# Kernel optimization log

Measured on AMD Instinct MI355X. Metric: run time of the kernel, lower is better.

## Reference

```python
import jax, jax.numpy as jnp
import numpy as np

D_MODEL = 1024
N_HEADS = 16
SEQ_LEN = 2048
BATCH = 2
NEG = -1.0e9


def sinusoidal_embeddings(seq_len, d_k):
    # Faithful to the torch version: row 0 is all zeros; even cols get sin,
    # odd cols get cos of position/theta (theta uses the SAME index j, not j//2).
    theta = 10000.0 ** (2.0 * jnp.arange(d_k, dtype=jnp.float32) / d_k)  # [d_k]
    pos = jnp.arange(1, seq_len, dtype=jnp.float32)[:, None] / theta      # [S-1, d_k]
    even = (jnp.arange(d_k) % 2 == 0)
    body = jnp.where(even, jnp.sin(pos), jnp.cos(pos))                    # [S-1, d_k]
    return jnp.concatenate([jnp.zeros((1, d_k), dtype=pos.dtype), body], axis=0)


def setup_inputs() -> dict:
    key = jax.random.key(0)
    k_x, k_q, k_k, k_v, k_o = jax.random.split(key, 5)
    scale = 0.02
    return {
        "X": jax.random.normal(k_x, (BATCH, SEQ_LEN, D_MODEL), dtype=jnp.float32),
        "W_q": jax.random.normal(k_q, (D_MODEL, D_MODEL), dtype=jnp.float32) * scale,
        "W_k": jax.random.normal(k_k, (D_MODEL, D_MODEL), dtype=jnp.float32) * scale,
        "W_v": jax.random.normal(k_v, (D_MODEL, D_MODEL), dtype=jnp.float32) * scale,
        "W_o": jax.random.normal(k_o, (D_MODEL, D_MODEL), dtype=jnp.float32) * scale,
    }


def reference(X, W_q, W_k, W_v, W_o):
    B, S, D = X.shape
    H, d_k = N_HEADS, D // N_HEADS

    def proj(W):  # nn.Linear (no bias): y = x @ W.T, then split heads -> [B,H,S,d_k]
        return (X @ W.T).reshape(B, S, H, d_k).transpose(0, 2, 1, 3)

    Q, K, V = proj(W_q), proj(W_k), proj(W_v)

    pos = sinusoidal_embeddings(S, d_k)          # [S, d_k]
    Q = Q + pos
    K = K + pos

    mask = jnp.triu(jnp.full((S, S), NEG, dtype=X.dtype), k=1)  # [S,S]
    scores = jnp.einsum("bhqd,bhkd->bhqk", Q, K) / jnp.sqrt(jnp.float32(d_k)) + mask
    weights = jax.nn.softmax(scores, axis=-1)
    attn = jnp.einsum("bhqk,bhkd->bhqd", weights, V)            # [B,H,S,d_k]

    attn = attn.transpose(0, 2, 1, 3).reshape(B, S, D)
    return attn @ W_o.T + X
```

## Files before the change

kernel.cpp:

```cpp
#include <hip/hip_runtime.h>
#include <hip/hip_bf16.h>
#include <math.h>

#define S_LEN 2048
#define DMODEL 1024
#define NHEADS 16
#define DHEAD 64
#define NBATCH 2
#define MROWS (NBATCH * S_LEN)

typedef float f32x4 __attribute__((ext_vector_type(4)));
typedef unsigned short u16x8 __attribute__((ext_vector_type(8)));
typedef __bf16 bf16x8 __attribute__((ext_vector_type(8)));

__device__ __forceinline__ f32x4 mfma16(u16x8 a, u16x8 b, f32x4 c) {
    return __builtin_amdgcn_mfma_f32_16x16x32_bf16(
        __builtin_bit_cast(bf16x8, a), __builtin_bit_cast(bf16x8, b), c, 0, 0, 0);
}

__device__ __forceinline__ unsigned short f2bf(float f) {
    unsigned int u = __builtin_bit_cast(unsigned int, f);
    u += 0x7FFFu + ((u >> 16) & 1u);
    return (unsigned short)(u >> 16);
}

__device__ __forceinline__ unsigned int cvtpk(float lo, float hi) {
    unsigned int r;
    asm("v_cvt_pk_bf16_f32 %0, %1, %2" : "=v"(r) : "v"(lo), "v"(hi));
    return r;
}

__device__ __forceinline__ void gl16(const void* g, void* l) {
    __builtin_amdgcn_global_load_lds(
        (const __attribute__((address_space(1))) unsigned int*)g,
        (__attribute__((address_space(3))) unsigned int*)l, 16, 0, 0);
}

#define VMB(N) do { \
    asm volatile("s_waitcnt vmcnt(" #N ")" ::: "memory"); \
    __builtin_amdgcn_sched_barrier(0); \
    __builtin_amdgcn_s_barrier(); \
    __builtin_amdgcn_sched_barrier(0); } while (0)

__global__ __launch_bounds__(256) void cvt5(
    const float* __restrict__ X, const float* __restrict__ Wq,
    const float* __restrict__ Wk, const float* __restrict__ Wv,
    const float* __restrict__ Wo,
    unsigned short* __restrict__ Xbf, unsigned short* __restrict__ Wbf,
    float* __restrict__ pos)
{
    int b = blockIdx.x;
    if (b >= 4096) {
        int i = (b - 4096) * 256 + threadIdx.x;
        int s = i >> 6, d = i & 63;
        float theta = powf(10000.0f, (2.0f * (float)d) / 64.0f);
        float x = (float)s / theta;
        float v = (d & 1) ? cosf(x) : sinf(x);
        pos[i] = (s == 0) ? 0.0f : v;
        return;
    }
    const float* s; unsigned short* d; int t;
    if (b < 2048) { s = X; d = Xbf; t = b * 256 + threadIdx.x; }
    else {
        int z = (b - 2048) >> 9, bb = (b - 2048) & 511;
        s = (z == 0) ? Wq : (z == 1) ? Wk : (z == 2) ? Wv : Wo;
        d = Wbf + (z << 20);
        t = bb * 256 + threadIdx.x;
    }
    float4 a = *((const float4*)s + t * 2);
    float4 c = *((const float4*)s + t * 2 + 1);
    u16x8 o;
    o[0] = f2bf(a.x); o[1] = f2bf(a.y); o[2] = f2bf(a.z); o[3] = f2bf(a.w);
    o[4] = f2bf(c.x); o[5] = f2bf(c.y); o[6] = f2bf(c.z); o[7] = f2bf(c.w);
    *((u16x8*)d + t) = o;
}

__global__ __launch_bounds__(512) void gemm_qkv(
    const unsigned short* __restrict__ Xbf, const unsigned short* __restrict__ Wbf,
    const float* __restrict__ pos,
    unsigned short* __restrict__ qb, unsigned short* __restrict__ kb,
    unsigned short* __restrict__ vt)
{
    __shared__ unsigned short L[2][28672];
    const int t = threadIdx.x;
    const int lane = t & 63;
    const int w = t >> 6;
    const int wm = w >> 2, wn = w & 3;
    const int m0 = blockIdx.x * 256;
    const int nb = blockIdx.y * 192;
    const int ll = lane & 15, lg = lane >> 4;
    const int tr = t >> 3;
    const int ch = (t & 7) ^ (tr & 7);

    f32x4 acc[8][3] = {};

    const unsigned short* gA[4];
    const unsigned short* gB[3];
    #pragma unroll
    for (int i = 0; i < 4; i++)
        gA[i] = Xbf + (m0 + i * 64 + tr) * 1024 + ch * 8;
    #pragma unroll
    for (int i = 0; i < 3; i++)
        gB[i] = Wbf + (nb + i * 64 + tr) * 1024 + ch * 8;

    const int sw0 = ((0 * 4 + lg) ^ (ll & 7)) * 16;
    const int sw1 = ((1 * 4 + lg) ^ (ll & 7)) * 16;
    const int aBase = (wm * 128 + ll) * 128;
    const int bBase = 32768 + (wn * 48 + ll) * 128;
    const int wdst = w * 8 * 64;

    auto stB01 = [&](unsigned short* Ln) {
        gl16(gB[0], Ln + 16384 + wdst);          gB[0] += 64;
        gl16(gB[1], Ln + 16384 + 4096 + wdst);   gB[1] += 64;
    };
    auto stB2 = [&](unsigned short* Ln) {
        gl16(gB[2], Ln + 16384 + 8192 + wdst);   gB[2] += 64;
    };
    auto stA02 = [&](unsigned short* Ln) {
        gl16(gA[0], Ln + wdst);                  gA[0] += 64;
        gl16(gA[2], Ln + 8192 + wdst);           gA[2] += 64;
    };
    auto stA13 = [&](unsigned short* Ln) {
        gl16(gA[1], Ln + 4096 + wdst);           gA[1] += 64;
        gl16(gA[3], Ln + 12288 + wdst);          gA[3] += 64;
    };

    u16x8 bf[3][2];
    auto loadB = [&](const char* bB) {
        #pragma unroll
        for (int nf = 0; nf < 3; nf++) {
            const char* p = bB + bBase + nf * 2048;
            bf[nf][0] = *(const u16x8*)(p + sw0);
            bf[nf][1] = *(const u16x8*)(p + sw1);
        }
    };
    auto quad = [&](int q, const char* bA) {
        const char* pa = bA + aBase + q * 4096;
        u16x8 a00 = *(const u16x8*)(pa + sw0);
        u16x8 a01 = *(const u16x8*)(pa + sw1);
        u16x8 a10 = *(const u16x8*)(pa + 2048 + sw0);
        u16x8 a11 = *(const u16x8*)(pa + 2048 + sw1);
        __builtin_amdgcn_s_setprio(1);
        #pragma unroll
        for (int nf = 0; nf < 3; nf++) {
            acc[q * 2 + 0][nf] = mfma16(a00, bf[nf][0], acc[q * 2 + 0][nf]);
            acc[q * 2 + 1][nf] = mfma16(a10, bf[nf][0], acc[q * 2 + 1][nf]);
        }
        #pragma unroll
        for (int nf = 0; nf < 3; nf++) {
            acc[q * 2 + 0][nf] = mfma16(a01, bf[nf][1], acc[q * 2 + 0][nf]);
            acc[q * 2 + 1][nf] = mfma16(a11, bf[nf][1], acc[q * 2 + 1][nf]);
        }
        __builtin_amdgcn_s_setprio(0);
    };

    stB01(L[0]); stB2(L[0]); stA02(L[0]); stA13(L[0]);
    VMB(2);

    #pragma unroll 1
    for (int tt = 0; tt < 15; tt++) {
        const char* bA = (const char*)L[tt & 1];
        unsigned short* Ln = L[(tt + 1) & 1];
        stB01(Ln);
        loadB(bA);
        quad(0, bA);
        __builtin_amdgcn_s_barrier();
        stB2(Ln);
        quad(1, bA);
        __builtin_amdgcn_s_barrier();
        stA02(Ln);
        VMB(5);
        quad(2, bA);
        __builtin_amdgcn_s_barrier();
        stA13(Ln);
        quad(3, bA);
        VMB(2);
    }
    {
        const char* bA = (const char*)L[1];
        loadB(bA);
        quad(0, bA);
        __builtin_amdgcn_s_barrier();
        quad(1, bA);
        VMB(0);
        quad(2, bA);
        quad(3, bA);
    }

    #pragma unroll
    for (int nf = 0; nf < 3; nf++) {
        const int c = nb + wn * 48 + nf * 16 + ll;
        const int zz = c >> 10;
        const int lc = c & 1023;
        const int h = lc >> 6, d = lc & 63;
        if (zz == 2) {
            #pragma unroll
            for (int mf = 0; mf < 8; mf++) {
                const int row0 = m0 + wm * 128 + mf * 16 + lg * 4;
                const int b = row0 >> 11, s0 = row0 & 2047;
                unsigned long long pk =
                    (unsigned long long)cvtpk(acc[mf][nf][0], acc[mf][nf][1]) |
                    ((unsigned long long)cvtpk(acc[mf][nf][2], acc[mf][nf][3]) << 32);
                *(unsigned long long*)&vt[(((b * NHEADS + h) * 64) + d) * S_LEN + s0] = pk;
            }
        } else {
            unsigned short* const dst = (zz == 0) ? qb : kb;
            const float pscale = (zz == 0) ? 0.1803368801111244f : 1.0f;
            #pragma unroll
            for (int mf = 0; mf < 8; mf++) {
                #pragma unroll
                for (int r = 0; r < 4; r++) {
                    const int row = m0 + wm * 128 + mf * 16 + lg * 4 + r;
                    const int b = row >> 11, s = row & 2047;
                    float v = acc[mf][nf][r] + pos[s * 64 + d];
                    v *= pscale;
                    dst[(((b * NHEADS + h) * S_LEN) + s) * 64 + d] = f2bf(v);
                }
            }
        }
    }
}

__global__ __launch_bounds__(512, 4) void attn_kernel(
    const unsigned short* __restrict__ qb,
    const unsigned short* __restrict__ kb,
    const unsigned short* __restrict__ vt,
    unsigned short* __restrict__ attnb)
{
    __shared__ unsigned short Klds[2][128 * 64];
    __shared__ unsigned short Vlds[2][64 * 128];
    __shared__ unsigned short Plds[8][16 * 64];

    const int bh = blockIdx.x;
    const int x = blockIdx.y;
    const int qt = (x < 8) ? (15 - x) : (x - 8);

    const int lane = threadIdx.x & 63;
    const int w = threadIdx.x >> 6;
    const int lg = lane >> 4, ll = lane & 15;
    const int r8 = lane >> 3, ch = (lane & 7) ^ r8;
    const int r4 = lane >> 4, c16 = lane & 15;

    const unsigned short* Q = qb + bh * (S_LEN * 64);
    const unsigned short* K = kb + bh * (S_LEN * 64);
    const unsigned short* V = vt + bh * (64 * S_LEN);
    const int q0 = qt * 128 + w * 16;

    u16x8 qf0 = *(const u16x8*)(Q + (q0 + ll) * 64 + lg * 8);
    u16x8 qf1 = *(const u16x8*)(Q + (q0 + ll) * 64 + 32 + lg * 8);

    u16x8 ones;
    #pragma unroll
    for (int i = 0; i < 8; i++) ones[i] = 0x3F80;

    f32x4 o_acc[4] = {};
    f32x4 l_acc = {};

    const int sw0 = ((0 * 4 + lg) ^ (ll & 7)) * 16;
    const int sw1 = ((1 * 4 + lg) ^ (ll & 7)) * 16;
    const char* kb0p0 = (const char*)&Klds[0][0] + ll * 128 + sw0;
    const char* kb0p1 = (const char*)&Klds[0][0] + ll * 128 + sw1;
    const char* kb1p0 = (const char*)&Klds[1][0] + ll * 128 + sw0;
    const char* kb1p1 = (const char*)&Klds[1][0] + ll * 128 + sw1;
    const char* vb0p0 = (const char*)&Vlds[0][0] + ll * 256 + sw0;
    const char* vb0p1 = (const char*)&Vlds[0][0] + ll * 256 + sw1;
    const char* vb1p0 = (const char*)&Vlds[1][0] + ll * 256 + sw0;
    const char* vb1p1 = (const char*)&Vlds[1][0] + ll * 256 + sw1;
    const int E = (ll & 7) << 4;
    char* pwb = (char*)&Plds[w][0] + (((ll * 128) + lg * 8) ^ (E & 16));
    const int pw_o0 = 0 ^ (E & 96), pw_o1 = 32 ^ (E & 96);
    const int pw_o2 = 64 ^ (E & 96), pw_o3 = 96 ^ (E & 96);
    const char* pr0 = (const char*)&Plds[w][0] + ll * 128 + sw0;
    const char* pr1 = (const char*)&Plds[w][0] + ll * 128 + sw1;
    unsigned short* kd0 = &Klds[0][(w * 16) * 64];
    unsigned short* kd1 = &Klds[1][(w * 16) * 64];
    unsigned short* vd0 = &Vlds[0][(w * 8) * 128];
    unsigned short* vd1 = &Vlds[1][(w * 8) * 128];
    const unsigned short* gk  = K + (w * 16 + r8) * 64 + ch * 8;
    const unsigned short* gva = V + (w * 8 + r4) * S_LEN + ((c16 ^ r4) * 8);
    const unsigned short* gvb = V + (w * 8 + 4 + r4) * S_LEN + ((c16 ^ (4 + r4)) * 8);
    const int dthr = w * 16 + ll - lg * 4;

    auto stage2 = [&](unsigned short* kd, unsigned short* vd) {
        gl16(gk, kd);
        gl16(gk + 512, kd + 512);
        gl16(gva, vd);
        gl16(gvb, vd + 512);
        gk += 128 * 64;
        gva += 128;
        gvb += 128;
    };

    auto tile_body = [&](const char* kp0, const char* kp1,
                         const char* vp0, const char* vp1, bool masked, int thr) {
        f32x4 sc[4] = {};
        __builtin_amdgcn_s_setprio(1);
        #pragma unroll
        for (int f = 0; f < 4; f++) {
            const u16x8 kfa = *(const u16x8*)(kp0 + f * 2048);
            sc[f] = mfma16(kfa, qf0, sc[f]);
            const u16x8 kfb = *(const u16x8*)(kp1 + f * 2048);
            sc[f] = mfma16(kfb, qf1, sc[f]);
        }
        __builtin_amdgcn_s_setprio(0);
        if (masked) {
            #pragma unroll
            for (int f = 0; f < 4; f++)
                #pragma unroll
                for (int r = 0; r < 4; r++)
                    if (f * 16 + r > thr) sc[f][r] = -1.0e9f;
        }
        #pragma unroll
        for (int f = 0; f < 4; f++)
            #pragma unroll
            for (int r = 0; r < 4; r++)
                sc[f][r] = __builtin_amdgcn_exp2f(sc[f][r]);
        *(unsigned long long*)(pwb + pw_o0) =
            (unsigned long long)cvtpk(sc[0][0], sc[0][1]) | ((unsigned long long)cvtpk(sc[0][2], sc[0][3]) << 32);
        *(unsigned long long*)(pwb + pw_o1) =
            (unsigned long long)cvtpk(sc[1][0], sc[1][1]) | ((unsigned long long)cvtpk(sc[1][2], sc[1][3]) << 32);
        *(unsigned long long*)(pwb + pw_o2) =
            (unsigned long long)cvtpk(sc[2][0], sc[2][1]) | ((unsigned long long)cvtpk(sc[2][2], sc[2][3]) << 32);
        *(unsigned long long*)(pwb + pw_o3) =
            (unsigned long long)cvtpk(sc[3][0], sc[3][1]) | ((unsigned long long)cvtpk(sc[3][2], sc[3][3]) << 32);
        const u16x8 pf0 = *(const u16x8*)pr0;
        const u16x8 pf1 = *(const u16x8*)pr1;
        __builtin_amdgcn_s_setprio(1);
        #pragma unroll
        for (int f = 0; f < 4; f++) {
            o_acc[f] = mfma16(pf0, *(const u16x8*)(vp0 + f * 4096), o_acc[f]);
            o_acc[f] = mfma16(pf1, *(const u16x8*)(vp1 + f * 4096), o_acc[f]);
        }
        l_acc = mfma16(pf0, ones, l_acc);
        l_acc = mfma16(pf1, ones, l_acc);
        __builtin_amdgcn_s_setprio(0);
    };

    auto body128_full = [&](const char* kp0, const char* kp1,
                            const char* vp0, const char* vp1) {
        tile_body(kp0, kp1, vp0, vp1, false, 0);
        tile_body(kp0 + 8192, kp1 + 8192, vp0 + 128, vp1 + 128, false, 0);
    };
    auto body128_diag = [&](const char* kp0, const char* kp1,
                            const char* vp0, const char* vp1) {
        tile_body(kp0, kp1, vp0, vp1, true, dthr);
        if (w >= 4)
            tile_body(kp0 + 8192, kp1 + 8192, vp0 + 128, vp1 + 128, true, dthr - 64);
    };

    stage2(kd0, vd0);
    __syncthreads();

    int p = 0;
    while (p + 2 <= qt) {
        stage2(kd1, vd1);
        body128_full(kb0p0, kb0p1, vb0p0, vb0p1);
        __syncthreads();
        stage2(kd0, vd0);
        body128_full(kb1p0, kb1p1, vb1p0, vb1p1);
        __syncthreads();
        p += 2;
    }
    if (p < qt) {
        stage2(kd1, vd1);
        body128_full(kb0p0, kb0p1, vb0p0, vb0p1);
        __syncthreads();
        body128_diag(kb1p0, kb1p1, vb1p0, vb1p1);
    } else {
        body128_diag(kb0p0, kb0p1, vb0p0, vb0p1);
    }

    const int bb = bh >> 4, h = bh & 15;
    const float lr0 = 1.0f / l_acc[0];
    const float lr1 = 1.0f / l_acc[1];
    const float lr2 = 1.0f / l_acc[2];
    const float lr3 = 1.0f / l_acc[3];
    #pragma unroll
    for (int f = 0; f < 4; f++) {
        const int colbase = h * 64 + f * 16 + ll;
        attnb[(bb * S_LEN + q0 + lg * 4 + 0) * DMODEL + colbase] = f2bf(o_acc[f][0] * lr0);
        attnb[(bb * S_LEN + q0 + lg * 4 + 1) * DMODEL + colbase] = f2bf(o_acc[f][1] * lr1);
        attnb[(bb * S_LEN + q0 + lg * 4 + 2) * DMODEL + colbase] = f2bf(o_acc[f][2] * lr2);
        attnb[(bb * S_LEN + q0 + lg * 4 + 3) * DMODEL + colbase] = f2bf(o_acc[f][3] * lr3);
    }
}

__global__ __launch_bounds__(512) void gemm_out(
    const unsigned short* __restrict__ Abf,
    const unsigned short* __restrict__ Wbf,
    const float* __restrict__ X,
    float* __restrict__ out)
{
    const unsigned short* __restrict__ W = Wbf + (3u << 20);
    __shared__ unsigned short L[3][16384];
    const int t = threadIdx.x;
    const int lane = t & 63;
    const int w = t >> 6;
    const int wm = w >> 2, wn = w & 3;
    const int m0 = blockIdx.x * 128;
    const int n0 = blockIdx.y * 128;
    const int ll = lane & 15, lg = lane >> 4;
    const int tr = t >> 3;
    const int ch = (t & 7) ^ (tr & 7);

    f32x4 acc[4][2] = {};

    const unsigned short* gA[2];
    const unsigned short* gB[2];
    #pragma unroll
    for (int i = 0; i < 2; i++) {
        gA[i] = Abf + (m0 + i * 64 + tr) * 1024 + ch * 8;
        gB[i] = W + (n0 + i * 64 + tr) * 1024 + ch * 8;
    }

    const int sw0 = ((0 * 4 + lg) ^ (ll & 7)) * 16;
    const int sw1 = ((1 * 4 + lg) ^ (ll & 7)) * 16;
    const int aBase = (wm * 64 + ll) * 128;
    const int bBase = 16384 + (wn * 32 + ll) * 128;
    const int wdst = w * 8 * 64;

    auto stA0 = [&](unsigned short* Ln) { gl16(gA[0], Ln + wdst);        gA[0] += 64; };
    auto stA1 = [&](unsigned short* Ln) { gl16(gA[1], Ln + 4096 + wdst); gA[1] += 64; };
    auto stB0 = [&](unsigned short* Ln) { gl16(gB[0], Ln + 8192 + wdst); gB[0] += 64; };
    auto stB1 = [&](unsigned short* Ln) { gl16(gB[1], Ln + 12288 + wdst); gB[1] += 64; };

    u16x8 bfv[2][2];
    auto loadB = [&](const char* bb) {
        #pragma unroll
        for (int nf = 0; nf < 2; nf++) {
            const char* p = bb + bBase + nf * 2048;
            bfv[nf][0] = *(const u16x8*)(p + sw0);
            bfv[nf][1] = *(const u16x8*)(p + sw1);
        }
    };
    auto quad = [&](int mf, const char* bb) {
        const char* pa = bb + aBase + mf * 2048;
        u16x8 a0 = *(const u16x8*)(pa + sw0);
        u16x8 a1 = *(const u16x8*)(pa + sw1);
        __builtin_amdgcn_s_setprio(1);
        #pragma unroll
        for (int nf = 0; nf < 2; nf++)
            acc[mf][nf] = mfma16(a0, bfv[nf][0], acc[mf][nf]);
        #pragma unroll
        for (int nf = 0; nf < 2; nf++)
            acc[mf][nf] = mfma16(a1, bfv[nf][1], acc[mf][nf]);
        __builtin_amdgcn_s_setprio(0);
    };

    auto ktile = [&](const char* bb, unsigned short* Ln, bool stg) {
        if (stg) stA0(Ln);
        loadB(bb);
        quad(0, bb);
        __builtin_amdgcn_s_barrier();
        if (stg) stA1(Ln);
        quad(1, bb);
        __builtin_amdgcn_s_barrier();
        if (stg) stB0(Ln);
        quad(2, bb);
        __builtin_amdgcn_s_barrier();
        if (stg) stB1(Ln);
        quad(3, bb);
    };

    stA0(L[0]); stA1(L[0]); stB0(L[0]); stB1(L[0]);
    stA0(L[1]); stA1(L[1]); stB0(L[1]); stB1(L[1]);
    VMB(4);
    #pragma unroll 1
    for (int tt = 0; tt < 4; tt++) {
        ktile((const char*)L[0], L[2], true); VMB(4);
        ktile((const char*)L[1], L[0], true); VMB(4);
        ktile((const char*)L[2], L[1], true); VMB(4);
    }
    ktile((const char*)L[0], L[2], true); VMB(4);
    ktile((const char*)L[1], L[0], true); VMB(4);
    ktile((const char*)L[2], nullptr, false); VMB(0);
    ktile((const char*)L[0], nullptr, false);

    #pragma unroll
    for (int mf = 0; mf < 4; mf++)
        #pragma unroll
        for (int nf = 0; nf < 2; nf++)
            #pragma unroll
            for (int r = 0; r < 4; r++) {
                const int row = m0 + wm * 64 + mf * 16 + lg * 4 + r;
                const int col = n0 + wn * 32 + nf * 16 + ll;
                out[row * 1024 + col] = acc[mf][nf][r] + X[row * 1024 + col];
            }
}

extern "C" void kernel_launch(void* const* d_in, const int* in_sizes, int n_in,
                              void* d_out, int out_size, void* d_ws, size_t ws_size,
                              hipStream_t stream) {
    const float* X  = (const float*)d_in[0];
    const float* Wq = (const float*)d_in[1];
    const float* Wk = (const float*)d_in[2];
    const float* Wv = (const float*)d_in[3];
    const float* Wo = (const float*)d_in[4];
    float* out = (float*)d_out;

    char* ws = (char*)d_ws;
    float*          pos  = (float*)(ws);
    unsigned short* Xbf  = (unsigned short*)(ws + (512u << 10));
    unsigned short* Wbf  = (unsigned short*)(ws + (512u << 10) + (8u  << 20));
    unsigned short* qb   = (unsigned short*)(ws + (512u << 10) + (16u << 20));
    unsigned short* kb   = (unsigned short*)(ws + (512u << 10) + (24u << 20));
    unsigned short* vt   = (unsigned short*)(ws + (512u << 10) + (32u << 20));
    unsigned short* attb = Xbf;

    cvt5<<<dim3(4608), dim3(256), 0, stream>>>(X, Wq, Wk, Wv, Wo, Xbf, Wbf, pos);
    gemm_qkv<<<dim3(16, 16), dim3(512), 0, stream>>>(Xbf, Wbf, pos, qb, kb, vt);
    attn_kernel<<<dim3(32, 16), dim3(512), 0, stream>>>(qb, kb, vt, attb);
    gemm_out<<<dim3(32, 8), dim3(512), 0, stream>>>(attb, Wbf, X, out);
}
```

Measured before the change: 89.92 us.

## Retile QKV GEMM to 128x128 blocks with triple-buffered LDS pipeline

The fused QKV projection GEMM moves from 256x192 tiles (256 blocks) to 128x128 tiles (768 blocks), with each block confined to one of Q/K/V so the epilogue branch is uniform. The LDS staging goes from double to triple buffering, with two tiles prefetched ahead. This is meant to fill more compute units and overlap global loads better, at the cost of lower per-block data reuse and more global traffic for the operand tiles.

```diff
diff --git a/kernel.cpp b/kernel.cpp
--- a/kernel.cpp
+++ b/kernel.cpp
@@ -81,136 +81,119 @@
     unsigned short* __restrict__ qb, unsigned short* __restrict__ kb,
     unsigned short* __restrict__ vt)
 {
-    __shared__ unsigned short L[2][28672];
+    const int z = blockIdx.y >> 3;
+    const unsigned short* __restrict__ W = Wbf + (z << 20);
+    __shared__ unsigned short L[3][16384];
     const int t = threadIdx.x;
     const int lane = t & 63;
     const int w = t >> 6;
     const int wm = w >> 2, wn = w & 3;
-    const int m0 = blockIdx.x * 256;
-    const int nb = blockIdx.y * 192;
+    const int m0 = blockIdx.x * 128;
+    const int n0 = (blockIdx.y & 7) * 128;
     const int ll = lane & 15, lg = lane >> 4;
     const int tr = t >> 3;
     const int ch = (t & 7) ^ (tr & 7);
 
-    f32x4 acc[8][3] = {};
-
-    const unsigned short* gA[4];
-    const unsigned short* gB[3];
+    f32x4 acc[4][2] = {};
+
+    const unsigned short* gA[2];
+    const unsigned short* gB[2];
     #pragma unroll
-    for (int i = 0; i < 4; i++)
+    for (int i = 0; i < 2; i++) {
         gA[i] = Xbf + (m0 + i * 64 + tr) * 1024 + ch * 8;
-    #pragma unroll
-    for (int i = 0; i < 3; i++)
-        gB[i] = Wbf + (nb + i * 64 + tr) * 1024 + ch * 8;
+        gB[i] = W + (n0 + i * 64 + tr) * 1024 + ch * 8;
+    }
 
     const int sw0 = ((0 * 4 + lg) ^ (ll & 7)) * 16;
     const int sw1 = ((1 * 4 + lg) ^ (ll & 7)) * 16;
-    const int aBase = (wm * 128 + ll) * 128;
-    const int bBase = 32768 + (wn * 48 + ll) * 128;
+    const int aBase = (wm * 64 + ll) * 128;
+    const int bBase = 16384 + (wn * 32 + ll) * 128;
     const int wdst = w * 8 * 64;
 
-    auto stB01 = [&](unsigned short* Ln) {
-        gl16(gB[0], Ln + 16384 + wdst);          gB[0] += 64;
-        gl16(gB[1], Ln + 16384 + 4096 + wdst);   gB[1] += 64;
-    };
-    auto stB2 = [&](unsigned short* Ln) {
-        gl16(gB[2], Ln + 16384 + 8192 + wdst);   gB[2] += 64;
-    };
-    auto stA02 = [&](unsigned short* Ln) {
-        gl16(gA[0], Ln + wdst);                  gA[0] += 64;
-        gl16(gA[2], Ln + 8192 + wdst);           gA[2] += 64;
-    };
-    auto stA13 = [&](unsigned short* Ln) {
-        gl16(gA[1], Ln + 4096 + wdst);           gA[1] += 64;
-        gl16(gA[3], Ln + 12288 + wdst);          gA[3] += 64;
-    };
-
-    u16x8 bf[3][2];
-    auto loadB = [&](const char* bB) {
-        #pragma unroll
-        for (int nf = 0; nf < 3; nf++) {
-            const char* p = bB + bBase + nf * 2048;
-            bf[nf][0] = *(const u16x8*)(p + sw0);
-            bf[nf][1] = *(const u16x8*)(p + sw1);
-        }
-    };
-    auto quad = [&](int q, const char* bA) {
-        const char* pa = bA + aBase + q * 4096;
-        u16x8 a00 = *(const u16x8*)(pa + sw0);
-        u16x8 a01 = *(const u16x8*)(pa + sw1);
-        u16x8 a10 = *(const u16x8*)(pa + 2048 + sw0);
-        u16x8 a11 = *(const u16x8*)(pa + 2048 + sw1);
+    auto stA0 = [&](unsigned short* Ln) { gl16(gA[0], Ln + wdst);        gA[0] += 64; };
+    auto stA1 = [&](unsigned short* Ln) { gl16(gA[1], Ln + 4096 + wdst); gA[1] += 64; };
+    auto stB0 = [&](unsigned short* Ln) { gl16(gB[0], Ln + 8192 + wdst); gB[0] += 64; };
+    auto stB1 = [&](unsigned short* Ln) { gl16(gB[1], Ln + 12288 + wdst); gB[1] += 64; };
+
+    u16x8 bfv[2][2];
+    auto loadB = [&](const char* bb) {
+        #pragma unroll
+        for (int nf = 0; nf < 2; nf++) {
+            const char* p = bb + bBase + nf * 2048;
+            bfv[nf][0] = *(const u16x8*)(p + sw0);
+            bfv[nf][1] = *(const u16x8*)(p + sw1);
+        }
+    };
+    auto quad = [&](int mf, const char* bb) {
+        const char* pa = bb + aBase + mf * 2048;
+        u16x8 a0 = *(const u16x8*)(pa + sw0);
+        u16x8 a1 = *(const u16x8*)(pa + sw1);
         __builtin_amdgcn_s_setprio(1);
         #pragma unroll
-        for (int nf = 0; nf < 3; nf++) {
-            acc[q * 2 + 0][nf] = mfma16(a00, bf[nf][0], acc[q * 2 + 0][nf]);
-            acc[q * 2 + 1][nf] = mfma16(a10, bf[nf][0], acc[q * 2 + 1][nf]);
-        }
-        #pragma unroll
-        for (int nf = 0; nf < 3; nf++) {
-            acc[q * 2 + 0][nf] = mfma16(a01, bf[nf][1], acc[q * 2 + 0][nf]);
-            acc[q * 2 + 1][nf] = mfma16(a11, bf[nf][1], acc[q * 2 + 1][nf]);
-        }
+        for (int nf = 0; nf < 2; nf++)
+            acc[mf][nf] = mfma16(a0, bfv[nf][0], acc[mf][nf]);
+        #pragma unroll
+        for (int nf = 0; nf < 2; nf++)
+            acc[mf][nf] = mfma16(a1, bfv[nf][1], acc[mf][nf]);
         __builtin_amdgcn_s_setprio(0);
     };
 
-    stB01(L[0]); stB2(L[0]); stA02(L[0]); stA13(L[0]);
-    VMB(2);
-
+    auto ktile = [&](const char* bb, unsigned short* Ln, bool stg) {
+        if (stg) stA0(Ln);
+        loadB(bb);
+        quad(0, bb);
+        __builtin_amdgcn_s_barrier();
+        if (stg) stA1(Ln);
+        quad(1, bb);
+        __builtin_amdgcn_s_barrier();
+        if (stg) stB0(Ln);
+        quad(2, bb);
+        __builtin_amdgcn_s_barrier();
+        if (stg) stB1(Ln);
+        quad(3, bb);
+    };
+
+    stA0(L[0]); stA1(L[0]); stB0(L[0]); stB1(L[0]);
+    stA0(L[1]); stA1(L[1]); stB0(L[1]); stB1(L[1]);
+    VMB(4);
     #pragma unroll 1
-    for (int tt = 0; tt < 15; tt++) {
-        const char* bA = (const char*)L[tt & 1];
-        unsigned short* Ln = L[(tt + 1) & 1];
-        stB01(Ln);
-        loadB(bA);
-        quad(0, bA);
-        __builtin_amdgcn_s_barrier();
-        stB2(Ln);
-        quad(1, bA);
-        __builtin_amdgcn_s_barrier();
-        stA02(Ln);
-        VMB(5);
-        quad(2, bA);
-        __builtin_amdgcn_s_barrier();
-        stA13(Ln);
-        quad(3, bA);
-        VMB(2);
-    }
-    {
-        const char* bA = (const char*)L[1];
-        loadB(bA);
-        quad(0, bA);
-        __builtin_amdgcn_s_barrier();
-        quad(1, bA);
-        VMB(0);
-        quad(2, bA);
-        quad(3, bA);
-    }
-
-    #pragma unroll
-    for (int nf = 0; nf < 3; nf++) {
-        const int c = nb + wn * 48 + nf * 16 + ll;
-        const int zz = c >> 10;
-        const int lc = c & 1023;
-        const int h = lc >> 6, d = lc & 63;
-        if (zz == 2) {
+    for (int tt = 0; tt < 4; tt++) {
+        ktile((const char*)L[0], L[2], true); VMB(4);
+        ktile((const char*)L[1], L[0], true); VMB(4);
+        ktile((const char*)L[2], L[1], true); VMB(4);
+    }
+    ktile((const char*)L[0], L[2], true); VMB(4);
+    ktile((const char*)L[1], L[0], true); VMB(4);
+    ktile((const char*)L[2], nullptr, false); VMB(0);
+    ktile((const char*)L[0], nullptr, false);
+
+    if (z == 2) {
+        #pragma unroll
+        for (int mf = 0; mf < 4; mf++) {
+            const int row0 = m0 + wm * 64 + mf * 16 + lg * 4;
+            const int b = row0 >> 11, s0 = row0 & 2047;
             #pragma unroll
-            for (int mf = 0; mf < 8; mf++) {
-                const int row0 = m0 + wm * 128 + mf * 16 + lg * 4;
-                const int b = row0 >> 11, s0 = row0 & 2047;
+            for (int nf = 0; nf < 2; nf++) {
+                const int c = n0 + wn * 32 + nf * 16 + ll;
+                const int h = c >> 6, d = c & 63;
                 unsigned long long pk =
                     (unsigned long long)cvtpk(acc[mf][nf][0], acc[mf][nf][1]) |
                     ((unsigned long long)cvtpk(acc[mf][nf][2], acc[mf][nf][3]) << 32);
                 *(unsigned long long*)&vt[(((b * NHEADS + h) * 64) + d) * S_LEN + s0] = pk;
             }
-        } else {
-            unsigned short* const dst = (zz == 0) ? qb : kb;
-            const float pscale = (zz == 0) ? 0.1803368801111244f : 1.0f;
+        }
+    } else {
+        unsigned short* const dst = (z == 0) ? qb : kb;
+        const float pscale = (z == 0) ? 0.1803368801111244f : 1.0f;
+        #pragma unroll
+        for (int mf = 0; mf < 4; mf++) {
             #pragma unroll
-            for (int mf = 0; mf < 8; mf++) {
+            for (int nf = 0; nf < 2; nf++) {
+                const int c = n0 + wn * 32 + nf * 16 + ll;
+                const int h = c >> 6, d = c & 63;
                 #pragma unroll
                 for (int r = 0; r < 4; r++) {
-                    const int row = m0 + wm * 128 + mf * 16 + lg * 4 + r;
+                    const int row = m0 + wm * 64 + mf * 16 + lg * 4 + r;
                     const int b = row >> 11, s = row & 2047;
                     float v = acc[mf][nf][r] + pos[s * 64 + d];
                     v *= pscale;
@@ -508,7 +491,7 @@
     unsigned short* attb = Xbf;
 
     cvt5<<<dim3(4608), dim3(256), 0, stream>>>(X, Wq, Wk, Wv, Wo, Xbf, Wbf, pos);
-    gemm_qkv<<<dim3(16, 16), dim3(512), 0, stream>>>(Xbf, Wbf, pos, qb, kb, vt);
+    gemm_qkv<<<dim3(32, 24), dim3(512), 0, stream>>>(Xbf, Wbf, pos, qb, kb, vt);
     attn_kernel<<<dim3(32, 16), dim3(512), 0, stream>>>(qb, kb, vt, attb);
     gemm_out<<<dim3(32, 8), dim3(512), 0, stream>>>(attb, Wbf, X, out);
 }
```

Result: slower. 96.77 us (+7.6%).
